# Performance work log

Measured on AMD Instinct MI355X. Metric: run time of the kernel, lower is better.

## Reference

```python
import jax, jax.numpy as jnp
import numpy as np

N = 50000; E = 120000; FN = 64; EA = 16; R = 4; H = 4; HID = 128; L = 3
NIDS = 10001; IDE = 32; RED = 8; NG = 64; NC = 10; KH = 128; GRID = 5; ORD = 3
EDIM = EA + RED; FFH = 256; GK = GRID + ORD


def layernorm(x, w, b):
    m = x.mean(-1, keepdims=True)
    v = ((x - m) ** 2).mean(-1, keepdims=True)
    return (x - m) / jnp.sqrt(v + 1e-5) * w + b


def b_splines(x, grid, k):
    # x: (B, in); grid: (in, G + 2k + 1) -> bases: (B, in, G + k)
    xe = x[..., None]
    bases = ((xe >= grid[:, :-1]) & (xe < grid[:, 1:])).astype(x.dtype)
    for j in range(1, k + 1):
        bases = ((xe - grid[:, :-(j + 1)]) / (grid[:, j:-1] - grid[:, :-(j + 1)]) * bases[..., :-1]
                 + (grid[:, j + 1:] - xe) / (grid[:, j + 1:] - grid[:, 1:-j]) * bases[..., 1:])
    return bases


def kan_linear(x, bw, sw, sc, grid):
    base = jax.nn.silu(x) @ bw.T
    B = b_splines(x, grid, ORD)
    return base + jnp.einsum('big,oig->bo', B, sw * sc[..., None])


def make_grid(in_features):
    h = 2.0 / GRID
    g = np.arange(-ORD, GRID + ORD + 1) * h - 1.0
    return jnp.asarray(np.tile(g, (in_features, 1)), dtype=jnp.float32)


def setup_inputs():
    key = jax.random.key(0)
    ks = jax.random.split(key, 24)
    s = 0.02
    inp = {}
    inp['x'] = jax.random.normal(ks[0], (N, FN), jnp.float32)
    inp['edge_attr'] = jax.random.normal(ks[1], (E, EA), jnp.float32)
    inp['id_token'] = jax.random.randint(ks[2], (N,), 0, NIDS)
    inp['edge_index'] = jax.random.randint(ks[3], (2, E), 0, N)
    inp['edge_type'] = jax.random.randint(ks[4], (E,), 0, R)
    inp['batch'] = jnp.sort(jax.random.randint(ks[5], (N,), 0, NG))
    inp['id_emb_table'] = jax.random.normal(ks[6], (NIDS, IDE)) * s
    inp['in_proj_w'] = jax.random.normal(ks[7], (HID, FN + IDE)) * s
    inp['in_proj_b'] = jnp.zeros((HID,))
    inp['rel_emb'] = jax.random.normal(ks[8], (L, R, RED)) * s
    inp['lin_l_w'] = jax.random.normal(ks[9], (L, R, H * HID, HID)) * s
    inp['lin_l_b'] = jnp.zeros((L, R, H * HID))
    inp['lin_r_w'] = jax.random.normal(ks[10], (L, R, H * HID, HID)) * s
    inp['lin_r_b'] = jnp.zeros((L, R, H * HID))
    inp['lin_edge_w'] = jax.random.normal(ks[11], (L, R, H * HID, EDIM)) * s
    inp['att_w'] = jax.random.normal(ks[12], (L, R, H, HID)) * s
    inp['conv_bias'] = jnp.zeros((L, R, HID))
    inp['rel_gate'] = jnp.zeros((L, R))
    inp['norm1_w'] = jnp.ones((L, HID)); inp['norm1_b'] = jnp.zeros((L, HID))
    inp['norm2_w'] = jnp.ones((L, HID)); inp['norm2_b'] = jnp.zeros((L, HID))
    inp['ffn_w1'] = jax.random.normal(ks[13], (L, FFH, HID)) * s
    inp['ffn_b1'] = jnp.zeros((L, FFH))
    inp['ffn_w2'] = jax.random.normal(ks[14], (L, HID, FFH)) * s
    inp['ffn_b2'] = jnp.zeros((L, HID))
    inp['readout_norm_w'] = jnp.ones((2 * HID,)); inp['readout_norm_b'] = jnp.zeros((2 * HID,))
    inp['base_w1'] = jax.random.normal(ks[15], (KH, 2 * HID)) * s
    inp['spline_w1'] = jax.random.normal(ks[16], (KH, 2 * HID, GK)) * s
    inp['spline_scaler1'] = jnp.ones((KH, 2 * HID))
    inp['grid1'] = make_grid(2 * HID)
    inp['base_w2'] = jax.random.normal(ks[17], (NC, KH)) * s
    inp['spline_w2'] = jax.random.normal(ks[18], (NC, KH, GK)) * s
    inp['spline_scaler2'] = jnp.ones((NC, KH))
    inp['grid2'] = make_grid(KH)
    return inp


def reference(x, edge_attr, id_token, edge_index, edge_type, batch,
              id_emb_table, in_proj_w, in_proj_b, rel_emb,
              lin_l_w, lin_l_b, lin_r_w, lin_r_b, lin_edge_w, att_w, conv_bias,
              rel_gate, norm1_w, norm1_b, norm2_w, norm2_b,
              ffn_w1, ffn_b1, ffn_w2, ffn_b2, readout_norm_w, readout_norm_b,
              base_w1, spline_w1, spline_scaler1, grid1,
              base_w2, spline_w2, spline_scaler2, grid2):
    src, dst = edge_index[0], edge_index[1]
    h = jnp.concatenate([x, id_emb_table[id_token]], -1)
    h = jax.nn.silu(h @ in_proj_w.T + in_proj_b)  # input_proj (eval: no dropout)
    for l in range(L):
        gate = jax.nn.softmax(rel_gate[l])  # all relations present w.h.p.
        h_msg = jnp.zeros_like(h)
        for r in range(R):
            maskf = (edge_type == r).astype(h.dtype)
            ea = jnp.concatenate([edge_attr, jnp.broadcast_to(rel_emb[l, r], (E, RED))], -1)
            xl = (h @ lin_l_w[l, r].T + lin_l_b[l, r]).reshape(N, H, HID)
            xr = (h @ lin_r_w[l, r].T + lin_r_b[l, r]).reshape(N, H, HID)
            ee = (ea @ lin_edge_w[l, r].T).reshape(E, H, HID)
            sfeat = jax.nn.leaky_relu(xl[src] + xr[dst] + ee, negative_slope=0.2)
            logit = jnp.einsum('ehc,hc->eh', sfeat, att_w[l, r])
            logit = jnp.where(maskf[:, None] > 0, logit, -1e9)
            m = jax.ops.segment_max(logit, dst, num_segments=N)
            a = jnp.exp(logit - m[dst]) * maskf[:, None]
            den = jax.ops.segment_sum(a, dst, num_segments=N)
            a = a / jnp.where(den == 0, 1.0, den)[dst]
            out = jax.ops.segment_sum(a[:, :, None] * xl[src], dst, num_segments=N)
            out = out.mean(1) + conv_bias[l, r]  # concat=False -> head mean
            h_msg = h_msg + gate[r] * out
        h = layernorm(h + h_msg, norm1_w[l], norm1_b[l])
        f = jax.nn.silu(h @ ffn_w1[l].T + ffn_b1[l]) @ ffn_w2[l].T + ffn_b2[l]
        h = layernorm(h + f, norm2_w[l], norm2_b[l])
    cnt = jax.ops.segment_sum(jnp.ones((N,), h.dtype), batch, num_segments=NG)
    hmean = jax.ops.segment_sum(h, batch, num_segments=NG) / jnp.maximum(cnt, 1.0)[:, None]
    hmax = jax.ops.segment_max(h, batch, num_segments=NG)
    g = layernorm(jnp.concatenate([hmean, hmax], -1), readout_norm_w, readout_norm_b)
    z = kan_linear(g, base_w1, spline_w1, spline_scaler1, grid1)
    logits = kan_linear(z, base_w2, spline_w2, spline_scaler2, grid2)
    return logits
```

## Files before the change

### kernel.cpp

```cpp
#include <hip/hip_runtime.h>
#include <math.h>

#define NN 50000
#define NE 120000
#define FN 64
#define NEA 16
#define NR 4
#define NH 4
#define HID 128
#define NL 3
#define IDE 32
#define RED 8
#define NG 64
#define NC 10
#define KH 128
#define FFH 256
#define NBIN (NR * NN)
#define SCAN_BLK ((NBIN + 1023) / 1024)
#define CAPS 32768
#define CAPH 9216

typedef short bf16x8 __attribute__((ext_vector_type(8)));
typedef float f32x4 __attribute__((ext_vector_type(4)));

__device__ __forceinline__ unsigned short f2b(float f) {
  unsigned u = __float_as_uint(f);
  unsigned r = (u + 0x7FFFu + ((u >> 16) & 1u)) >> 16;
  return (unsigned short)r;
}
__device__ __forceinline__ float b2f(unsigned short b) {
  return __uint_as_float((unsigned)b << 16);
}

__global__ void cvt_bf16(const float* __restrict__ s, unsigned short* __restrict__ d, int n4) {
  int i = blockIdx.x * blockDim.x + threadIdx.x;
  if (i >= n4) return;
  float4 v = ((const float4*)s)[i];
  ushort4 o;
  o.x = f2b(v.x); o.y = f2b(v.y); o.z = f2b(v.z); o.w = f2b(v.w);
  ((ushort4*)d)[i] = o;
}

template <int KT>
__device__ __forceinline__ void gemm_direct(
    const unsigned short* __restrict__ A, const int* __restrict__ rowlist,
    const unsigned short* __restrict__ W, const float* __restrict__ bias,
    float* __restrict__ Cf, unsigned short* __restrict__ Cb,
    int nrows, int mout, int act, int rowBase, int colBase) {
  constexpr int NK = KT / 32;
  __shared__ unsigned short Es[64][136];
  int t = threadIdx.x;
  int lane = t & 63, w = t >> 6;
  int wm = w >> 1, wn = w & 1;
  int q = lane >> 4, mr = lane & 15;

  const unsigned short* ap[2];
#pragma unroll
  for (int mt = 0; mt < 2; ++mt) {
    int gr = rowBase + wm * 32 + mt * 16 + mr;
    int cg = (gr < nrows) ? gr : 0;
    int ar = rowlist ? rowlist[cg] : cg;
    ap[mt] = A + (size_t)ar * KT + q * 8;
  }
  const unsigned short* wp[4];
#pragma unroll
  for (int nt = 0; nt < 4; ++nt)
    wp[nt] = W + (size_t)(colBase + wn * 64 + nt * 16 + mr) * KT + q * 8;

  f32x4 acc[2][4] = {};
#pragma unroll
  for (int k = 0; k < NK; ++k) {
    bf16x8 af[2], bfr[4];
#pragma unroll
    for (int mt = 0; mt < 2; ++mt) af[mt] = *(const bf16x8*)(ap[mt] + k * 32);
#pragma unroll
    for (int nt = 0; nt < 4; ++nt) bfr[nt] = *(const bf16x8*)(wp[nt] + k * 32);
#pragma unroll
    for (int mt = 0; mt < 2; ++mt)
#pragma unroll
      for (int nt = 0; nt < 4; ++nt)
        acc[mt][nt] = __builtin_amdgcn_mfma_f32_16x16x32_bf16(af[mt], bfr[nt], acc[mt][nt], 0, 0, 0);
  }

  float bv[4];
#pragma unroll
  for (int nt = 0; nt < 4; ++nt) bv[nt] = bias[colBase + wn * 64 + nt * 16 + mr];

  if (Cf) {
#pragma unroll
    for (int mt = 0; mt < 2; ++mt)
#pragma unroll
      for (int nt = 0; nt < 4; ++nt)
#pragma unroll
        for (int r = 0; r < 4; ++r) {
          int row = rowBase + wm * 32 + mt * 16 + q * 4 + r;
          int col = colBase + wn * 64 + nt * 16 + mr;
          if (row < nrows) {
            float v = acc[mt][nt][r] + bv[nt];
            if (act) v = v / (1.f + expf(-v));
            Cf[(size_t)row * mout + col] = v;
            if (Cb) Cb[(size_t)row * mout + col] = f2b(v);
          }
        }
  } else {
#pragma unroll
    for (int mt = 0; mt < 2; ++mt)
#pragma unroll
      for (int nt = 0; nt < 4; ++nt)
#pragma unroll
        for (int r = 0; r < 4; ++r) {
          float v = acc[mt][nt][r] + bv[nt];
          if (act) v = v / (1.f + expf(-v));
          Es[wm * 32 + mt * 16 + q * 4 + r][wn * 64 + nt * 16 + mr] = f2b(v);
        }
    __syncthreads();
    int rl = t >> 2, co = (t & 3) * 32;
    int grow = rowBase + rl;
    if (grow < nrows) {
      unsigned short* dst = Cb + (size_t)grow * mout + colBase + co;
#pragma unroll
      for (int j = 0; j < 4; ++j)
        *(bf16x8*)(dst + j * 8) = *(const bf16x8*)&Es[rl][co + j * 8];
    }
  }
}

template <int KT>
__global__ __launch_bounds__(256, 2) void gemm_bf16_t(
    const unsigned short* __restrict__ A, const unsigned short* __restrict__ W,
    const float* __restrict__ bias, float* __restrict__ Cf, unsigned short* __restrict__ Cb,
    int nrows, int mout, int act, int ncol) {
  int nbr = (nrows + 63) >> 6;
  int rpx = (nbr + 7) >> 3;
  int xcd = blockIdx.x & 7, j = blockIdx.x >> 3;
  int rowT = xcd * rpx + j / ncol;
  int cy = j - (j / ncol) * ncol;
  if (rowT >= nbr) return;
  gemm_direct<KT>(A, nullptr, W, bias, Cf, Cb, nrows, mout, act, rowT * 64, cy * 128);
}

__global__ __launch_bounds__(256, 2) void conv_solo_all(
    const unsigned short* __restrict__ hbf,
    const int* __restrict__ srclist, const int* __restrict__ hotlist,
    const int* __restrict__ cnts,
    const unsigned short* __restrict__ Wl, const float* __restrict__ bl,
    const unsigned short* __restrict__ Wr, const float* __restrict__ br,
    unsigned short* __restrict__ xlb, unsigned short* __restrict__ xrh,
    const int* __restrict__ solosrc, const int* __restrict__ solodst,
    const unsigned short* __restrict__ wsum, const float* __restrict__ bsum,
    const float* __restrict__ gate, float* __restrict__ hacc) {
  int t = threadIdx.x, lane = t & 63, w = t >> 6;
  int wm = w >> 1, wn = w & 1, q = lane >> 4, mr = lane & 15;
  for (int tid = blockIdx.x;; tid += gridDim.x) {
    int rem = tid, seg = 0, nrows = 0;
    for (; seg < 12; ++seg) {
      int n, tseg;
      if (seg < 8) {
        int r = seg >> 1;
        n = (seg & 1) ? cnts[64 + r * 16] : cnts[128 + r * 16];
        int cap = (seg & 1) ? CAPH : CAPS;
        if (n > cap) n = cap;
        tseg = ((n + 63) >> 6) * 4;
      } else {
        n = cnts[(seg - 8) * 16];
        tseg = (n + 63) >> 6;
      }
      if (rem < tseg) { nrows = n; break; }
      rem -= tseg;
    }
    if (seg == 12) return;
    if (seg < 8) {
      int r = seg >> 1, sel = seg & 1;
      int rt = rem >> 2, ct = rem & 3;
      const int* list = (sel ? hotlist : srclist) + r * NN;
      const unsigned short* W = (sel ? Wr : Wl) + (size_t)r * 512 * 128;
      const float* bias = (sel ? br : bl) + (size_t)r * 512;
      unsigned short* C = sel ? (xrh + (size_t)r * CAPH * 512) : (xlb + (size_t)r * CAPS * 512);
      gemm_direct<128>(hbf, list, W, bias, nullptr, C, nrows, 512, 0, rt * 64, ct * 128);
    } else {
      int r = seg - 8;
      int rowBase = rem * 64;
      const unsigned short* ap[2];
#pragma unroll
      for (int mt = 0; mt < 2; ++mt) {
        int gr = rowBase + wm * 32 + mt * 16 + mr;
        int idx = (gr < nrows) ? solosrc[r * NN + gr] : 0;
        ap[mt] = hbf + (size_t)idx * HID + q * 8;
      }
      const unsigned short* wp[4];
#pragma unroll
      for (int nt = 0; nt < 4; ++nt)
        wp[nt] = wsum + (size_t)r * 16384 + (size_t)(wn * 64 + nt * 16 + mr) * HID + q * 8;
      f32x4 acc[2][4] = {};
#pragma unroll
      for (int k = 0; k < 4; ++k) {
        bf16x8 af[2], bfr[4];
#pragma unroll
        for (int mt = 0; mt < 2; ++mt) af[mt] = *(const bf16x8*)(ap[mt] + k * 32);
#pragma unroll
        for (int nt = 0; nt < 4; ++nt) bfr[nt] = *(const bf16x8*)(wp[nt] + k * 32);
#pragma unroll
        for (int mt = 0; mt < 2; ++mt)
#pragma unroll
          for (int nt = 0; nt < 4; ++nt)
            acc[mt][nt] = __builtin_amdgcn_mfma_f32_16x16x32_bf16(af[mt], bfr[nt], acc[mt][nt], 0, 0, 0);
      }
      float g4 = gate[r] * 0.25f;
      float bv[4];
#pragma unroll
      for (int nt = 0; nt < 4; ++nt) bv[nt] = bsum[r * 128 + wn * 64 + nt * 16 + mr];
#pragma unroll
      for (int mt = 0; mt < 2; ++mt)
#pragma unroll
        for (int rr = 0; rr < 4; ++rr) {
          int row = rowBase + wm * 32 + mt * 16 + q * 4 + rr;
          if (row < nrows) {
            int dst = solodst[r * NN + row];
#pragma unroll
            for (int nt = 0; nt < 4; ++nt) {
              int col = wn * 64 + nt * 16 + mr;
              atomicAdd(&hacc[(size_t)dst * HID + col], g4 * (acc[mt][nt][rr] + bv[nt]));
            }
          }
        }
    }
    __syncthreads();
  }
}

__global__ void wsum_build(const float* __restrict__ linlw, const float* __restrict__ linlb,
                           unsigned short* __restrict__ wsum, float* __restrict__ bsum) {
  int i = blockIdx.x * blockDim.x + threadIdx.x;
  if (i >= NL * NR * 128 * 128) return;
  int k = i & 127, o = (i >> 7) & 127, lr = i >> 14;
  float s = 0.f;
#pragma unroll
  for (int h = 0; h < NH; ++h) s += linlw[((size_t)lr * 512 + h * 128 + o) * 128 + k];
  wsum[i] = f2b(s);
  if (k == 0) {
    float b = 0.f;
#pragma unroll
    for (int h = 0; h < NH; ++h) b += linlb[(size_t)lr * 512 + h * 128 + o];
    bsum[lr * 128 + o] = b;
  }
}

__global__ __launch_bounds__(256, 2) void layer_tail(
    float* __restrict__ h, const float* __restrict__ cb,
    const float* __restrict__ n1w, const float* __restrict__ n1b,
    const unsigned short* __restrict__ W1, const float* __restrict__ b1,
    const unsigned short* __restrict__ W2, const float* __restrict__ b2,
    const float* __restrict__ n2w, const float* __restrict__ n2b,
    unsigned short* __restrict__ hbfout) {
  __shared__ __align__(16) char smem[64 * 136 * 2 + 64 * 264 * 2];
  unsigned short (*Y)[136] = (unsigned short (*)[136])smem;
  unsigned short (*F1)[264] = (unsigned short (*)[264])(smem + 64 * 136 * 2);
  float (*Ef)[132] = (float (*)[132])(smem + 64 * 136 * 2);
  int nbr = (NN + 63) >> 6;
  int rpx = (nbr + 7) >> 3;
  int xcd = blockIdx.x & 7, j = blockIdx.x >> 3;
  int rowT = xcd * rpx + j;
  if (rowT >= nbr) return;
  int rowBase = rowT * 64;

  int t = threadIdx.x;
  int lane = t & 63, w = t >> 6;
  int wm = w >> 1, wn = w & 1;
  int q = lane >> 4, mr = lane & 15;

  float y0r[16], y1r[16];
  {
    float w0 = n1w[lane], w1 = n1w[64 + lane];
    float bb0 = n1b[lane], bb1 = n1b[64 + lane];
    float c0 = cb[lane], c1 = cb[64 + lane];
#pragma unroll
    for (int it = 0; it < 16; ++it) {
      int rr = it * 4 + w;
      int grow = rowBase + rr;
      if (grow < NN) {
        size_t base = (size_t)grow * HID;
        float x0 = h[base + lane] + c0;
        float x1 = h[base + 64 + lane] + c1;
        float s = x0 + x1;
#pragma unroll
        for (int o = 32; o > 0; o >>= 1) s += __shfl_xor(s, o, 64);
        float mean = s * (1.f / 128.f);
        float d0 = x0 - mean, d1 = x1 - mean;
        float v = d0 * d0 + d1 * d1;
#pragma unroll
        for (int o = 32; o > 0; o >>= 1) v += __shfl_xor(v, o, 64);
        float inv = 1.f / sqrtf(v * (1.f / 128.f) + 1e-5f);
        float y0 = d0 * inv * w0 + bb0;
        float y1 = d1 * inv * w1 + bb1;
        y0r[it] = y0;
        y1r[it] = y1;
        Y[rr][lane] = f2b(y0);
        Y[rr][64 + lane] = f2b(y1);
      } else {
        y0r[it] = 0.f;
        y1r[it] = 0.f;
        Y[rr][lane] = 0;
        Y[rr][64 + lane] = 0;
      }
    }
  }
  __syncthreads();

  bf16x8 a[2][4];
#pragma unroll
  for (int mt = 0; mt < 2; ++mt)
#pragma unroll
    for (int k = 0; k < 4; ++k)
      a[mt][k] = *(const bf16x8*)&Y[wm * 32 + mt * 16 + mr][k * 32 + q * 8];

#pragma unroll
  for (int ph = 0; ph < 2; ++ph) {
    const unsigned short* wp[4];
#pragma unroll
    for (int nt = 0; nt < 4; ++nt)
      wp[nt] = W1 + (size_t)(ph * 128 + wn * 64 + nt * 16 + mr) * HID + q * 8;
    f32x4 acc[2][4] = {};
#pragma unroll
    for (int k = 0; k < 4; ++k) {
      bf16x8 bfr[4];
#pragma unroll
      for (int nt = 0; nt < 4; ++nt) bfr[nt] = *(const bf16x8*)(wp[nt] + k * 32);
#pragma unroll
      for (int mt = 0; mt < 2; ++mt)
#pragma unroll
        for (int nt = 0; nt < 4; ++nt)
          acc[mt][nt] = __builtin_amdgcn_mfma_f32_16x16x32_bf16(a[mt][k], bfr[nt], acc[mt][nt], 0, 0, 0);
    }
    float bv[4];
#pragma unroll
    for (int nt = 0; nt < 4; ++nt) bv[nt] = b1[ph * 128 + wn * 64 + nt * 16 + mr];
#pragma unroll
    for (int mt = 0; mt < 2; ++mt)
#pragma unroll
      for (int nt = 0; nt < 4; ++nt)
#pragma unroll
        for (int r = 0; r < 4; ++r) {
          float v = acc[mt][nt][r] + bv[nt];
          v = v / (1.f + expf(-v));
          F1[wm * 32 + mt * 16 + q * 4 + r][ph * 128 + wn * 64 + nt * 16 + mr] = f2b(v);
        }
  }
  __syncthreads();

  const unsigned short* wp2[4];
#pragma unroll
  for (int nt = 0; nt < 4; ++nt)
    wp2[nt] = W2 + (size_t)(wn * 64 + nt * 16 + mr) * FFH + q * 8;
  f32x4 acc2[2][4] = {};
#pragma unroll
  for (int k = 0; k < 8; ++k) {
    bf16x8 af[2], bfr[4];
#pragma unroll
    for (int mt = 0; mt < 2; ++mt)
      af[mt] = *(const bf16x8*)&F1[wm * 32 + mt * 16 + mr][k * 32 + q * 8];
#pragma unroll
    for (int nt = 0; nt < 4; ++nt) bfr[nt] = *(const bf16x8*)(wp2[nt] + k * 32);
#pragma unroll
    for (int mt = 0; mt < 2; ++mt)
#pragma unroll
      for (int nt = 0; nt < 4; ++nt)
        acc2[mt][nt] = __builtin_amdgcn_mfma_f32_16x16x32_bf16(af[mt], bfr[nt], acc2[mt][nt], 0, 0, 0);
  }
  __syncthreads();

  float bv2[4];
#pragma unroll
  for (int nt = 0; nt < 4; ++nt) bv2[nt] = b2[wn * 64 + nt * 16 + mr];
#pragma unroll
  for (int mt = 0; mt < 2; ++mt)
#pragma unroll
    for (int nt = 0; nt < 4; ++nt)
#pragma unroll
      for (int r = 0; r < 4; ++r)
        Ef[wm * 32 + mt * 16 + q * 4 + r][wn * 64 + nt * 16 + mr] = acc2[mt][nt][r] + bv2[nt];
  __syncthreads();

  float w0 = n2w[lane], w1 = n2w[64 + lane];
  float bb0 = n2b[lane], bb1 = n2b[64 + lane];
#pragma unroll
  for (int it = 0; it < 16; ++it) {
    int rr = it * 4 + w;
    int grow = rowBase + rr;
    if (grow >= NN) continue;
    size_t base = (size_t)grow * HID;
    float x0 = y0r[it] + Ef[rr][lane];
    float x1 = y1r[it] + Ef[rr][64 + lane];
    float s = x0 + x1;
#pragma unroll
    for (int o = 32; o > 0; o >>= 1) s += __shfl_xor(s, o, 64);
    float mean = s * (1.f / 128.f);
    float d0 = x0 - mean, d1 = x1 - mean;
    float v = d0 * d0 + d1 * d1;
#pragma unroll
    for (int o = 32; o > 0; o >>= 1) v += __shfl_xor(v, o, 64);
    float inv = 1.f / sqrtf(v * (1.f / 128.f) + 1e-5f);
    float y0 = d0 * inv * w0 + bb0;
    float y1 = d1 * inv * w1 + bb1;
    h[base + lane] = y0;
    h[base + 64 + lane] = y1;
    hbfout[base + lane] = f2b(y0);
    hbfout[base + 64 + lane] = f2b(y1);
  }
}

__global__ void build_xin_bf(const float* __restrict__ x, const int* __restrict__ idtok,
                             const float* __restrict__ emb, unsigned short* __restrict__ xin) {
  int i = blockIdx.x * blockDim.x + threadIdx.x;
  if (i >= NN * 96) return;
  int n = i / 96, k = i - n * 96;
  float v = (k < FN) ? x[(size_t)n * FN + k] : emb[(size_t)idtok[n] * IDE + (k - FN)];
  xin[i] = f2b(v);
}

__global__ void hist_bin(const int* __restrict__ ei, const int* __restrict__ et,
                         int* __restrict__ bcnt) {
  int e = blockIdx.x * blockDim.x + threadIdx.x;
  if (e >= NE) return;
  atomicAdd(&bcnt[et[e] * NN + ei[NE + e]], 1);
}
__global__ __launch_bounds__(256) void scan1(const int* __restrict__ cnt,
                                             int* __restrict__ pos, int* __restrict__ bsum) {
  __shared__ int lds[256];
  int b = blockIdx.x, t = threadIdx.x;
  int base = b * 1024 + t * 4;
  int v[4];
#pragma unroll
  for (int j = 0; j < 4; ++j) v[j] = (base + j < NBIN) ? cnt[base + j] : 0;
  int tot = v[0] + v[1] + v[2] + v[3];
  lds[t] = tot;
  __syncthreads();
  for (int off = 1; off < 256; off <<= 1) {
    int x = (t >= off) ? lds[t - off] : 0;
    __syncthreads();
    lds[t] += x;
    __syncthreads();
  }
  if (t == 255) bsum[b] = lds[255];
  int run = lds[t] - tot;
#pragma unroll
  for (int j = 0; j < 4; ++j) {
    if (base + j < NBIN) pos[base + j] = run;
    run += v[j];
  }
}
__global__ __launch_bounds__(256) void scan2(int* __restrict__ bsum) {
  __shared__ int lds[256];
  int t = threadIdx.x;
  int v = (t < SCAN_BLK) ? bsum[t] : 0;
  lds[t] = v;
  __syncthreads();
  for (int off = 1; off < 256; off <<= 1) {
    int x = (t >= off) ? lds[t - off] : 0;
    __syncthreads();
    lds[t] += x;
    __syncthreads();
  }
  if (t < SCAN_BLK) bsum[t] = lds[t] - v;
}
__global__ void scan3(int* __restrict__ pos, const int* __restrict__ bsum,
                      const int* __restrict__ cnt) {
  int i = blockIdx.x * blockDim.x + threadIdx.x;
  if (i >= NBIN) return;
  pos[i] += bsum[i >> 10];
  if (i == NBIN - 1) pos[NBIN] = pos[i] + cnt[i];
}
__global__ void scatter_bin(const int* __restrict__ ei, const int* __restrict__ et,
                            const int* __restrict__ csroff, int* __restrict__ cur,
                            int* __restrict__ elist) {
  int e = blockIdx.x * blockDim.x + threadIdx.x;
  if (e >= NE) return;
  int bin = et[e] * NN + ei[NE + e];
  int p = atomicAdd(&cur[bin], 1);
  elist[csroff[bin] + p] = e;
}
__global__ void sort_bins(const int* __restrict__ csroff, int* __restrict__ elist) {
  int b = blockIdx.x * blockDim.x + threadIdx.x;
  if (b >= NBIN) return;
  int s = csroff[b], e = csroff[b + 1];
  for (int i = s + 1; i < e; ++i) {
    int key = elist[i];
    int j = i - 1;
    while (j >= s && elist[j] > key) { elist[j + 1] = elist[j]; --j; }
    elist[j + 1] = key;
  }
}
__global__ void gather_edge(const int* __restrict__ ei, const int* __restrict__ et,
                            const int* __restrict__ elist, const int* __restrict__ csroff,
                            const float* __restrict__ eattr,
                            int* __restrict__ rsrc, float* __restrict__ eacsr,
                            int* __restrict__ srcflag) {
  int p = blockIdx.x * blockDim.x + threadIdx.x;
  if (p >= NE) return;
  int e = elist[p];
  int src = ei[e];
  rsrc[p] = src;
  const float4* s = (const float4*)(eattr + (size_t)e * NEA);
  float4* d = (float4*)(eacsr + (size_t)p * NEA);
#pragma unroll
  for (int j = 0; j < 4; ++j) d[j] = s[j];
  int bin = et[e] * NN + ei[NE + e];
  if (csroff[bin + 1] - csroff[bin] >= 2) srcflag[et[e] * NN + src] = 1;
}
__global__ void build_src_o(const int* __restrict__ srcflag, const int* __restrict__ srcpos,
                            int* __restrict__ srclist, int* __restrict__ srcmap) {
  int b = blockIdx.x * blockDim.x + threadIdx.x;
  if (b >= NBIN) return;
  if (srcflag[b]) {
    int rel = b / NN;
    int pos = srcpos[b] - srcpos[rel * NN];
    srcmap[b] = pos;
    srclist[rel * NN + pos] = b - rel * NN;
  }
}
__global__ void fincnt(const int* __restrict__ srcpos, int* __restrict__ nsrc) {
  int r = threadIdx.x;
  if (r < NR) nsrc[r * 16] = srcpos[(r + 1) * NN] - srcpos[r * NN];
}
__global__ void remap_rsrc(const int* __restrict__ csroff, const int* __restrict__ rsrc,
                           const int* __restrict__ srcmap, int* __restrict__ rsrcx) {
  int p = blockIdx.x * blockDim.x + threadIdx.x;
  if (p >= NE) return;
  int rel = (p >= csroff[NN]) + (p >= csroff[2 * NN]) + (p >= csroff[3 * NN]);
  rsrcx[p] = srcmap[rel * NN + rsrc[p]];
}
__global__ __launch_bounds__(256) void build_hot(
    const int* __restrict__ csroff, const int* __restrict__ rsrc,
    int* __restrict__ nsolo, int* __restrict__ nhot,
    int* __restrict__ solosrc, int* __restrict__ solodst, int* __restrict__ hotlist) {
  __shared__ int wsc[4][4], whc[4][4];
  __shared__ int sbase[4], hbase[4];
  int t = threadIdx.x, wave = t >> 6, lane = t & 63;
  int b = blockIdx.x * 256 + t;
  bool valid = b < NBIN;
  int cnt = 0, rel = 0, s = 0;
  if (valid) { s = csroff[b]; cnt = csroff[b + 1] - s; rel = b / NN; }
  bool solo = valid && cnt == 1;
  bool hot = valid && cnt >= 2;
#pragma unroll
  for (int rr = 0; rr < 4; ++rr) {
    unsigned long long ms = __ballot(solo && rel == rr);
    unsigned long long mh = __ballot(hot && rel == rr);
    if (lane == 0) { wsc[wave][rr] = __popcll(ms); whc[wave][rr] = __popcll(mh); }
  }
  __syncthreads();
  if (t < 4) {
    int ssum = wsc[0][t] + wsc[1][t] + wsc[2][t] + wsc[3][t];
    int hsum = whc[0][t] + whc[1][t] + whc[2][t] + whc[3][t];
    sbase[t] = ssum ? atomicAdd(&nsolo[t * 16], ssum) : 0;
    hbase[t] = hsum ? atomicAdd(&nhot[t * 16], hsum) : 0;
  }
  __syncthreads();
#pragma unroll
  for (int rr = 0; rr < 4; ++rr) {
    unsigned long long ms = __ballot(solo && rel == rr);
    if (solo && rel == rr) {
      int before = 0;
#pragma unroll
      for (int wv = 0; wv < 4; ++wv) if (wv < wave) before += wsc[wv][rr];
      int pos = sbase[rr] + before + __popcll(ms & ((1ull << lane) - 1ull));
      solosrc[rr * NN + pos] = rsrc[s];
      solodst[rr * NN + pos] = b - rr * NN;
    }
    unsigned long long mh = __ballot(hot && rel == rr);
    if (hot && rel == rr) {
      int before = 0;
#pragma unroll
      for (int wv = 0; wv < 4; ++wv) if (wv < wave) before += whc[wv][rr];
      int pos = hbase[rr] + before + __popcll(mh & ((1ull << lane) - 1ull));
      hotlist[rr * NN + pos] = b - rr * NN;
    }
  }
}

__global__ void gate_cb_all(const float* __restrict__ rg, const float* __restrict__ cbias,
                            float* __restrict__ gate, float* __restrict__ cb) {
  __shared__ float g[NR];
  int l = blockIdx.x, t = threadIdx.x;
  const float* rgl = rg + l * NR;
  if (t == 0) {
    float mx = rgl[0];
    for (int r = 1; r < NR; ++r) mx = fmaxf(mx, rgl[r]);
    float s = 0.f, tmp[NR];
    for (int r = 0; r < NR; ++r) { tmp[r] = expf(rgl[r] - mx); s += tmp[r]; }
    for (int r = 0; r < NR; ++r) { g[r] = tmp[r] / s; gate[l * NR + r] = g[r]; }
  }
  __syncthreads();
  float c = 0.f;
  for (int r = 0; r < NR; ++r) c += g[r] * cbias[(size_t)l * NR * HID + r * HID + t];
  cb[l * HID + t] = c;
}

__global__ __launch_bounds__(256) void edge_merged(
    const int* __restrict__ csroff, const int* __restrict__ rsrcx,
    const float* __restrict__ eacsr, const float* __restrict__ relembL,
    const float* __restrict__ wedgeL, const float* __restrict__ attwL,
    const unsigned short* __restrict__ xlb, const unsigned short* __restrict__ xrh,
    const int* __restrict__ hotlist, const int* __restrict__ nhot,
    float* __restrict__ hacc, const float* __restrict__ gate) {
  __shared__ float lds[4][128];
  int wave = threadIdx.x >> 6, lane = threadIdx.x & 63;
  int rel = blockIdx.x & 3;
  int b0 = blockIdx.x >> 2;
  int bstride = gridDim.x >> 2;
  float g4 = gate[rel] * 0.25f;
  int hh = wave;
  const float* wedgep = wedgeL + (size_t)rel * 512 * 24;
  const float* attwp = attwL + (size_t)rel * 512;
  const float* relembp = relembL + rel * RED;
  const unsigned short* xlbase = xlb + (size_t)rel * CAPS * 512;
  const unsigned short* xrbase = xrh + (size_t)rel * CAPH * 512;
  float wreg[2][24], areg[2];
#pragma unroll
  for (int j = 0; j < 2; ++j) {
    int col = hh * 128 + j * 64 + lane;
    const float* wp = wedgep + (size_t)col * 24;
#pragma unroll
    for (int k = 0; k < 24; ++k) wreg[j][k] = wp[k];
    areg[j] = attwp[col];
  }
  float evr0 = 0.f, evr1 = 0.f;
#pragma unroll
  for (int k = 0; k < 8; ++k) {
    float rk = relembp[k];
    evr0 += rk * wreg[0][NEA + k];
    evr1 += rk * wreg[1][NEA + k];
  }
  int nh = nhot[rel * 16];
  for (int wi = b0; wi < nh; wi += bstride) {
    int dst = hotlist[rel * NN + wi];
    int s = csroff[rel * NN + dst], e = csroff[rel * NN + dst + 1];
    {
      const unsigned short* xrp = xrbase + (size_t)wi * 512;
      float xr0 = b2f(xrp[hh * 128 + lane]);
      float xr1 = b2f(xrp[hh * 128 + 64 + lane]);
      float m = -3.4e38f, den = 0.f, acc0 = 0.f, acc1 = 0.f;
      for (int p = s; p < e; ++p) {
        int src = rsrcx[p];
        const float* eap = eacsr + (size_t)p * NEA;
        float eev0 = evr0, eev1 = evr1;
#pragma unroll
        for (int k = 0; k < NEA; ++k) {
          float er = eap[k];
          eev0 += er * wreg[0][k];
          eev1 += er * wreg[1][k];
        }
        float xl0 = b2f(xlbase[(size_t)src * 512 + hh * 128 + lane]);
        float xl1 = b2f(xlbase[(size_t)src * 512 + hh * 128 + 64 + lane]);
        float s0 = xl0 + xr0 + eev0; s0 = (s0 > 0.f) ? s0 : 0.2f * s0;
        float s1 = xl1 + xr1 + eev1; s1 = (s1 > 0.f) ? s1 : 0.2f * s1;
        float lg = s0 * areg[0] + s1 * areg[1];
#pragma unroll
        for (int o = 32; o > 0; o >>= 1) lg += __shfl_xor(lg, o, 64);
        float mn = fmaxf(m, lg);
        float sc = expf(m - mn);
        float ex = expf(lg - mn);
        den = den * sc + ex;
        acc0 = acc0 * sc + ex * xl0;
        acc1 = acc1 * sc + ex * xl1;
        m = mn;
      }
      float wgt = g4 / den;
      lds[wave][lane] = acc0 * wgt;
      lds[wave][64 + lane] = acc1 * wgt;
    }
    __syncthreads();
    if (wave < 2) {
      int d = wave * 64 + lane;
      float v = lds[0][d] + lds[1][d] + lds[2][d] + lds[3][d];
      atomicAdd(&hacc[(size_t)dst * HID + d], v);
    }
    __syncthreads();
  }
}

__global__ void group_bounds(const int* __restrict__ batch, int* __restrict__ gstart) {
  int g = threadIdx.x + blockIdx.x * blockDim.x;
  if (g > NG) return;
  int lo = 0, hi = NN;
  while (lo < hi) {
    int mid = (lo + hi) >> 1;
    if (batch[mid] < g) lo = mid + 1; else hi = mid;
  }
  gstart[g] = lo;
}
__global__ __launch_bounds__(128) void readout_part2(
    const float* __restrict__ h, const int* __restrict__ gstart,
    float* __restrict__ psum, float* __restrict__ pmax) {
  int g = blockIdx.x, s = blockIdx.y, t = threadIdx.x;
  int r0 = gstart[g], r1 = gstart[g + 1];
  float acc = 0.f, mx = -3.4e38f;
  for (int row = r0 + s; row < r1; row += 8) {
    float v = h[(size_t)row * HID + t];
    acc += v;
    mx = fmaxf(mx, v);
  }
  psum[((size_t)g * 8 + s) * HID + t] = acc;
  pmax[((size_t)g * 8 + s) * HID + t] = mx;
}
__global__ __launch_bounds__(256) void readout_final(
    const int* __restrict__ gstart, const float* __restrict__ psum,
    const float* __restrict__ pmax, const float* __restrict__ w,
    const float* __restrict__ b, float* __restrict__ g) {
  int bg = blockIdx.x, t = threadIdx.x;
  __shared__ float red[256];
  float c = fmaxf((float)(gstart[bg + 1] - gstart[bg]), 1.f);
  float x;
  if (t < HID) {
    float ssum = 0.f;
    for (int s = 0; s < 8; ++s) ssum += psum[((size_t)bg * 8 + s) * HID + t];
    x = ssum / c;
  } else {
    float mx = -3.4e38f;
    for (int s = 0; s < 8; ++s) mx = fmaxf(mx, pmax[((size_t)bg * 8 + s) * HID + (t - HID)]);
    x = mx;
  }
  red[t] = x;
  __syncthreads();
  for (int s = 128; s > 0; s >>= 1) {
    if (t < s) red[t] += red[t + s];
    __syncthreads();
  }
  float mean = red[0] * (1.f / 256.f);
  __syncthreads();
  float d = x - mean;
  red[t] = d * d;
  __syncthreads();
  for (int s = 128; s > 0; s >>= 1) {
    if (t < s) red[t] += red[t + s];
    __syncthreads();
  }
  float inv = 1.f / sqrtf(red[0] * (1.f / 256.f) + 1e-5f);
  g[(size_t)bg * 256 + t] = d * inv * w[t] + b[t];
}

__device__ __forceinline__ void bspline8(float x, const float* __restrict__ t,
                                         float* __restrict__ out) {
  float bs[11];
#pragma unroll
  for (int j = 0; j < 11; ++j) bs[j] = (x >= t[j] && x < t[j + 1]) ? 1.f : 0.f;
#pragma unroll
  for (int k = 1; k <= 3; ++k) {
    for (int j = 0; j < 11 - k; ++j) {
      bs[j] = (x - t[j]) / (t[j + k] - t[j]) * bs[j] +
              (t[j + k + 1] - x) / (t[j + k + 1] - t[j + 1]) * bs[j + 1];
    }
  }
#pragma unroll
  for (int j = 0; j < 8; ++j) out[j] = bs[j];
}

__global__ __launch_bounds__(128) void kan1_part(
    const float* __restrict__ g, const float* __restrict__ bw,
    const float* __restrict__ sw, const float* __restrict__ sc,
    const float* __restrict__ grid, float* __restrict__ zpart) {
  int bg = blockIdx.x, ch = blockIdx.y, t = threadIdx.x;
  int base = ch * 32;
  __shared__ float B[32][8];
  __shared__ float sg[32];
  if (t < 32) {
    float x = g[(size_t)bg * 256 + base + t];
    sg[t] = x / (1.f + expf(-x));
    bspline8(x, grid + (size_t)(base + t) * 12, B[t]);
  }
  __syncthreads();
  float acc = 0.f;
  for (int i = 0; i < 32; ++i) {
    int col = base + i;
    acc += sg[i] * bw[(size_t)t * 256 + col];
    const float* swp = sw + ((size_t)t * 256 + col) * 8;
    float sp = 0.f;
#pragma unroll
    for (int k = 0; k < 8; ++k) sp += B[i][k] * swp[k];
    acc += sp * sc[(size_t)t * 256 + col];
  }
  zpart[((size_t)ch * NG + bg) * KH + t] = acc;
}

__global__ __launch_bounds__(128) void kan2(
    const float* __restrict__ zpart, const float* __restrict__ bw,
    const float* __restrict__ sw, const float* __restrict__ sc,
    const float* __restrict__ grid, float* __restrict__ out) {
  int bg = blockIdx.x, t = threadIdx.x;
  __shared__ float B[128][8];
  __shared__ float sz[128];
  float x = 0.f;
  for (int ch = 0; ch < 8; ++ch) x += zpart[((size_t)ch * NG + bg) * KH + t];
  sz[t] = x / (1.f + expf(-x));
  bspline8(x, grid + (size_t)t * 12, B[t]);
  __syncthreads();
  if (t < NC) {
    float acc = 0.f;
    for (int i = 0; i < 128; ++i) {
      acc += sz[i] * bw[(size_t)t * 128 + i];
      const float* swp = sw + ((size_t)t * 128 + i) * 8;
      float sp = 0.f;
#pragma unroll
      for (int k = 0; k < 8; ++k) sp += B[i][k] * swp[k];
      acc += sp * sc[(size_t)t * 128 + i];
    }
    out[(size_t)bg * NC + t] = acc;
  }
}

extern "C" void kernel_launch(void* const* d_in, const int* in_sizes, int n_in,
                              void* d_out, int out_size, void* d_ws, size_t ws_size,
                              hipStream_t stream) {
  const float* x       = (const float*)d_in[0];
  const float* eattr   = (const float*)d_in[1];
  const int*   idtok   = (const int*)d_in[2];
  const int*   ei      = (const int*)d_in[3];
  const int*   etype   = (const int*)d_in[4];
  const int*   batch   = (const int*)d_in[5];
  const float* idemb   = (const float*)d_in[6];
  const float* inw     = (const float*)d_in[7];
  const float* inb     = (const float*)d_in[8];
  const float* relemb  = (const float*)d_in[9];
  const float* linlw   = (const float*)d_in[10];
  const float* linlb   = (const float*)d_in[11];
  const float* linrw   = (const float*)d_in[12];
  const float* linrb   = (const float*)d_in[13];
  const float* linew   = (const float*)d_in[14];
  const float* attw    = (const float*)d_in[15];
  const float* convb   = (const float*)d_in[16];
  const float* relgate = (const float*)d_in[17];
  const float* n1w     = (const float*)d_in[18];
  const float* n1b     = (const float*)d_in[19];
  const float* n2w     = (const float*)d_in[20];
  const float* n2b     = (const float*)d_in[21];
  const float* f1w     = (const float*)d_in[22];
  const float* f1bias  = (const float*)d_in[23];
  const float* f2w     = (const float*)d_in[24];
  const float* f2bias  = (const float*)d_in[25];
  const float* rnw     = (const float*)d_in[26];
  const float* rnb     = (const float*)d_in[27];
  const float* bw1     = (const float*)d_in[28];
  const float* sw1     = (const float*)d_in[29];
  const float* sc1     = (const float*)d_in[30];
  const float* grid1   = (const float*)d_in[31];
  const float* bw2     = (const float*)d_in[32];
  const float* sw2     = (const float*)d_in[33];
  const float* sc2     = (const float*)d_in[34];
  const float* grid2   = (const float*)d_in[35];
  float* out = (float*)d_out;
  (void)in_sizes; (void)n_in; (void)out_size; (void)ws_size;

  char* p = (char*)d_ws;
  auto alloc = [&](size_t bytes) { void* q = (void*)p; p += (bytes + 255) & ~(size_t)255; return q; };
  float* h    = (float*)alloc((size_t)NN * HID * 4);
  unsigned short* hbf = (unsigned short*)alloc((size_t)NN * HID * 2);
  unsigned short* xlb = (unsigned short*)alloc((size_t)NR * CAPS * 512 * 2);
  unsigned short* xrh = (unsigned short*)alloc((size_t)NR * CAPH * 512 * 2);
  int* elist = (int*)alloc((size_t)NE * 4);
  int* rsrc  = (int*)alloc((size_t)NE * 4);
  int* rsrcx = (int*)alloc((size_t)NE * 4);
  float* eacsr = (float*)alloc((size_t)NE * NEA * 4);
  int* bcnt  = (int*)alloc((size_t)NBIN * 8 + 8);
  int* cur   = bcnt + NBIN;
  int* csroff = (int*)alloc((size_t)(NBIN + 1) * 4);
  int* srcpos = (int*)alloc((size_t)(NBIN + 1) * 4);
  int* bsum  = (int*)alloc((size_t)SCAN_BLK * 4);
  int* hotlist = (int*)alloc((size_t)NR * NN * 4);
  int* solosrc = (int*)alloc((size_t)NR * NN * 4);
  int* solodst = (int*)alloc((size_t)NR * NN * 4);
  int* srclist = (int*)alloc((size_t)NR * NN * 4);
  int* srcflag = (int*)alloc((size_t)NBIN * 4);
  int* srcmap  = (int*)alloc((size_t)NBIN * 4);
  int* cnts    = (int*)alloc(1024);
  int* nsolo   = cnts;
  int* nhot    = cnts + 64;
  int* nsrc    = cnts + 128;
  unsigned short* linlwb = (unsigned short*)alloc((size_t)NL * NR * 512 * 128 * 2);
  unsigned short* linrwb = (unsigned short*)alloc((size_t)NL * NR * 512 * 128 * 2);
  unsigned short* f1wb   = (unsigned short*)alloc((size_t)NL * 256 * 128 * 2);
  unsigned short* f2wb   = (unsigned short*)alloc((size_t)NL * 128 * 256 * 2);
  unsigned short* inwb   = (unsigned short*)alloc((size_t)128 * 96 * 2);
  unsigned short* wsumb  = (unsigned short*)alloc((size_t)NL * NR * 128 * 128 * 2);
  float* bsumf = (float*)alloc((size_t)NL * NR * 128 * 4);
  float* gate = (float*)alloc(NL * NR * 4);
  float* cb   = (float*)alloc(NL * HID * 4);
  int* gstart = (int*)alloc((size_t)(NG + 1) * 4);
  float* psum = (float*)alloc((size_t)NG * 8 * HID * 4);
  float* pmax = (float*)alloc((size_t)NG * 8 * HID * 4);
  float* zpart = (float*)alloc((size_t)8 * NG * KH * 4);
  float* g = (float*)alloc((size_t)NG * 256 * 4);
  unsigned short* xinbf = xlb;

  const int NB64 = (NN + 63) / 64;
  const int RPX = (NB64 + 7) / 8;

  {
    int n;
    n = NL * NR * 512 * 128 / 4;
    cvt_bf16<<<(n + 255) / 256, 256, 0, stream>>>(linlw, linlwb, n);
    cvt_bf16<<<(n + 255) / 256, 256, 0, stream>>>(linrw, linrwb, n);
    n = NL * 256 * 128 / 4;
    cvt_bf16<<<(n + 255) / 256, 256, 0, stream>>>(f1w, f1wb, n);
    cvt_bf16<<<(n + 255) / 256, 256, 0, stream>>>(f2w, f2wb, n);
    n = 128 * 96 / 4;
    cvt_bf16<<<(n + 255) / 256, 256, 0, stream>>>(inw, inwb, n);
  }
  wsum_build<<<(NL * NR * 128 * 128 + 255) / 256, 256, 0, stream>>>(linlw, linlb, wsumb, bsumf);

  hipMemsetAsync(bcnt, 0, (size_t)NBIN * 8 + 8, stream);
  hipMemsetAsync(srcflag, 0, (size_t)NBIN * 4, stream);
  hipMemsetAsync(cnts, 0, 1024, stream);
  hist_bin<<<(NE + 255) / 256, 256, 0, stream>>>(ei, etype, bcnt);
  scan1<<<SCAN_BLK, 256, 0, stream>>>(bcnt, csroff, bsum);
  scan2<<<1, 256, 0, stream>>>(bsum);
  scan3<<<(NBIN + 255) / 256, 256, 0, stream>>>(csroff, bsum, bcnt);
  scatter_bin<<<(NE + 255) / 256, 256, 0, stream>>>(ei, etype, csroff, cur, elist);
  sort_bins<<<(NBIN + 255) / 256, 256, 0, stream>>>(csroff, elist);
  gather_edge<<<(NE + 255) / 256, 256, 0, stream>>>(ei, etype, elist, csroff, eattr,
                                                    rsrc, eacsr, srcflag);
  scan1<<<SCAN_BLK, 256, 0, stream>>>(srcflag, srcpos, bsum);
  scan2<<<1, 256, 0, stream>>>(bsum);
  scan3<<<(NBIN + 255) / 256, 256, 0, stream>>>(srcpos, bsum, srcflag);
  build_src_o<<<(NBIN + 255) / 256, 256, 0, stream>>>(srcflag, srcpos, srclist, srcmap);
  fincnt<<<1, 64, 0, stream>>>(srcpos, nsrc);
  remap_rsrc<<<(NE + 255) / 256, 256, 0, stream>>>(csroff, rsrc, srcmap, rsrcx);
  build_hot<<<(NBIN + 255) / 256, 256, 0, stream>>>(csroff, rsrc, nsolo, nhot,
                                                    solosrc, solodst, hotlist);
  gate_cb_all<<<NL, 128, 0, stream>>>(relgate, convb, gate, cb);

  build_xin_bf<<<(NN * 96 + 255) / 256, 256, 0, stream>>>(x, idtok, idemb, xinbf);
  gemm_bf16_t<96><<<8 * RPX, 256, 0, stream>>>(xinbf, inwb, inb, h, hbf, NN, 128, 1, 1);

  for (int l = 0; l < NL; ++l) {
    conv_solo_all<<<4096, 256, 0, stream>>>(
        hbf, srclist, hotlist, cnts,
        linlwb + (size_t)l * NR * 512 * 128, linlb + (size_t)l * NR * 512,
        linrwb + (size_t)l * NR * 512 * 128, linrb + (size_t)l * NR * 512,
        xlb, xrh,
        solosrc, solodst,
        wsumb + (size_t)l * NR * 16384, bsumf + (size_t)l * NR * 128,
        gate + l * NR, h);
    edge_merged<<<4096, 256, 0, stream>>>(
        csroff, rsrcx, eacsr,
        relemb + (size_t)l * NR * RED,
        linew + (size_t)l * NR * 512 * 24,
        attw + (size_t)l * NR * 512,
        xlb, xrh, hotlist, nhot, h, gate + l * NR);
    layer_tail<<<8 * RPX, 256, 0, stream>>>(
        h, cb + l * HID, n1w + l * HID, n1b + l * HID,
        f1wb + (size_t)l * 256 * 128, f1bias + (size_t)l * 256,
        f2wb + (size_t)l * 128 * 256, f2bias + (size_t)l * 128,
        n2w + l * HID, n2b + l * HID, hbf);
  }

  group_bounds<<<1, 128, 0, stream>>>(batch, gstart);
  readout_part2<<<dim3(NG, 8), 128, 0, stream>>>(h, gstart, psum, pmax);
  readout_final<<<NG, 256, 0, stream>>>(gstart, psum, pmax, rnw, rnb, g);
  kan1_part<<<dim3(NG, 8), 128, 0, stream>>>(g, bw1, sw1, sc1, grid1, zpart);
  kan2<<<NG, 128, 0, stream>>>(zpart, bw2, sw2, sc2, grid2, out);
}
```

Before: 962.6 us.

## Load gathered A rows once and loop over all output column tiles in-block

In the relation conv GEMM, each block now gathers its 64 input rows once into registers and loops over all four 128-column output tiles, instead of launching four separate tiles that each re-gather the same rows. This removes redundant indirect gathers of hbf and list lookups. The trade-off is fewer, longer tasks, which lowers parallelism, and more register pressure from holding the A fragments. The syncthreads placement is also adjusted so the shared staging buffer can be reused across iterations.

```diff
diff --git a/kernel.cpp b/kernel.cpp
--- a/kernel.cpp
+++ b/kernel.cpp
@@ -122,6 +122,7 @@
       for (int j = 0; j < 4; ++j)
         *(bf16x8*)(dst + j * 8) = *(const bf16x8*)&Es[rl][co + j * 8];
     }
+    __syncthreads();
   }
 }
 
@@ -149,6 +150,7 @@
     const int* __restrict__ solosrc, const int* __restrict__ solodst,
     const unsigned short* __restrict__ wsum, const float* __restrict__ bsum,
     const float* __restrict__ gate, float* __restrict__ hacc) {
+  __shared__ unsigned short Es[64][136];
   int t = threadIdx.x, lane = t & 63, w = t >> 6;
   int wm = w >> 1, wn = w & 1, q = lane >> 4, mr = lane & 15;
   for (int tid = blockIdx.x;; tid += gridDim.x) {
@@ -160,7 +162,7 @@
         n = (seg & 1) ? cnts[64 + r * 16] : cnts[128 + r * 16];
         int cap = (seg & 1) ? CAPH : CAPS;
         if (n > cap) n = cap;
-        tseg = ((n + 63) >> 6) * 4;
+        tseg = (n + 63) >> 6;
       } else {
         n = cnts[(seg - 8) * 16];
         tseg = (n + 63) >> 6;
@@ -171,12 +173,63 @@
     if (seg == 12) return;
     if (seg < 8) {
       int r = seg >> 1, sel = seg & 1;
-      int rt = rem >> 2, ct = rem & 3;
+      int rowBase = rem * 64;
       const int* list = (sel ? hotlist : srclist) + r * NN;
       const unsigned short* W = (sel ? Wr : Wl) + (size_t)r * 512 * 128;
       const float* bias = (sel ? br : bl) + (size_t)r * 512;
       unsigned short* C = sel ? (xrh + (size_t)r * CAPH * 512) : (xlb + (size_t)r * CAPS * 512);
-      gemm_direct<128>(hbf, list, W, bias, nullptr, C, nrows, 512, 0, rt * 64, ct * 128);
+      const unsigned short* ap[2];
+#pragma unroll
+      for (int mt = 0; mt < 2; ++mt) {
+        int gr = rowBase + wm * 32 + mt * 16 + mr;
+        int cg = (gr < nrows) ? gr : 0;
+        ap[mt] = hbf + (size_t)list[cg] * HID + q * 8;
+      }
+      bf16x8 a[2][4];
+#pragma unroll
+      for (int mt = 0; mt < 2; ++mt)
+#pragma unroll
+        for (int k = 0; k < 4; ++k) a[mt][k] = *(const bf16x8*)(ap[mt] + k * 32);
+#pragma unroll
+      for (int ct = 0; ct < 4; ++ct) {
+        const unsigned short* wp[4];
+#pragma unroll
+        for (int nt = 0; nt < 4; ++nt)
+          wp[nt] = W + (size_t)(ct * 128 + wn * 64 + nt * 16 + mr) * HID + q * 8;
+        f32x4 acc[2][4] = {};
+#pragma unroll
+        for (int k = 0; k < 4; ++k) {
+          bf16x8 bfr[4];
+#pragma unroll
+          for (int nt = 0; nt < 4; ++nt) bfr[nt] = *(const bf16x8*)(wp[nt] + k * 32);
+#pragma unroll
+          for (int mt = 0; mt < 2; ++mt)
+#pragma unroll
+            for (int nt = 0; nt < 4; ++nt)
+              acc[mt][nt] = __builtin_amdgcn_mfma_f32_16x16x32_bf16(a[mt][k], bfr[nt], acc[mt][nt], 0, 0, 0);
+        }
+        float bv[4];
+#pragma unroll
+        for (int nt = 0; nt < 4; ++nt) bv[nt] = bias[ct * 128 + wn * 64 + nt * 16 + mr];
+#pragma unroll
+        for (int mt = 0; mt < 2; ++mt)
+#pragma unroll
+          for (int nt = 0; nt < 4; ++nt)
+#pragma unroll
+            for (int rr = 0; rr < 4; ++rr)
+              Es[wm * 32 + mt * 16 + q * 4 + rr][wn * 64 + nt * 16 + mr] =
+                  f2b(acc[mt][nt][rr] + bv[nt]);
+        __syncthreads();
+        int rl = t >> 2, co = (t & 3) * 32;
+        int grow = rowBase + rl;
+        if (grow < nrows) {
+          unsigned short* dst = C + (size_t)grow * 512 + ct * 128 + co;
+#pragma unroll
+          for (int j = 0; j < 4; ++j)
+            *(bf16x8*)(dst + j * 8) = *(const bf16x8*)&Es[rl][co + j * 8];
+        }
+        __syncthreads();
+      }
     } else {
       int r = seg - 8;
       int rowBase = rem * 64;
@@ -223,8 +276,8 @@
             }
           }
         }
+      __syncthreads();
     }
-    __syncthreads();
   }
 }
 
```

New measurement: 942.3 us (median of 2 runs). 2.1% less time.
